# Optimization experiments

Hardware: AMD Instinct MI355X
Metric: run time of the kernel (lower is better)

Reference implementation:

```python
import jax, jax.numpy as jnp
import numpy as np

GRID = 8
SPACING = 2.0
RADIUS = 3.0
B = 64
CODE = 1024
HID = 128
L = 4
EPS = 1e-5


def _layernorm(h, g, b):
    mu = h.mean(-1, keepdims=True)
    var = ((h - mu) ** 2).mean(-1, keepdims=True)
    return (h - mu) * jax.lax.rsqrt(var + EPS) * g + b


def setup_inputs() -> dict:
    key = jax.random.key(0)
    ks = jax.random.split(key, 16)
    n = GRID ** 3
    # grid coords, centered, spacing=anchor_spacing (create_grid_coords)
    idx = np.arange(GRID)
    coords = (np.stack(np.meshgrid(idx, idx, idx, indexing='ij'), -1).reshape(-1, 3)
              - (GRID - 1) / 2.0) * SPACING
    # radius_graph per batch: identical geometry per graph -> offset base edges
    d2 = ((coords[:, None, :] - coords[None, :, :]) ** 2).sum(-1)
    mask = (d2 <= RADIUS ** 2) & (d2 > 0)
    r0, c0 = np.nonzero(mask)
    off = (np.arange(B) * n)[:, None]
    row = (r0[None, :] + off).reshape(-1)
    col = (c0[None, :] + off).reshape(-1)
    edge_index = jnp.asarray(np.stack([row, col]), dtype=jnp.int32)  # [2,E]
    grid_coords = jnp.asarray(np.tile(coords, (B, 1)), dtype=jnp.float32)  # [B*n,3]
    s = 0.02
    inp = {
        'y': jax.random.normal(ks[0], (B, n, CODE), jnp.float32),
        'grid_coords': grid_coords,
        'edge_index': edge_index,
        'W_in': jax.random.normal(ks[1], (HID, CODE), jnp.float32) * s,
        'b_in': jnp.zeros((HID,), jnp.float32),
        'gam': jnp.ones((L, HID), jnp.float32),
        'bet': jnp.zeros((L, HID), jnp.float32),
        'eW1': jax.random.normal(ks[2], (L, HID, 2 * HID + 1), jnp.float32) * s,
        'eb1': jnp.zeros((L, HID), jnp.float32),
        'eW2': jax.random.normal(ks[3], (L, HID, HID), jnp.float32) * s,
        'eb2': jnp.zeros((L, HID), jnp.float32),
        'nW1': jax.random.normal(ks[4], (L, HID, 2 * HID), jnp.float32) * s,
        'nb1': jnp.zeros((L, HID), jnp.float32),
        'nW2': jax.random.normal(ks[5], (L, HID, HID), jnp.float32) * s,
        'nb2': jnp.zeros((L, HID), jnp.float32),
        'W_out': jax.random.normal(ks[6], (CODE, HID), jnp.float32) * s,
        'b_out': jnp.zeros((CODE,), jnp.float32),
    }
    return inp


def reference(y, grid_coords, edge_index, W_in, b_in, gam, bet,
              eW1, eb1, eW2, eb2, nW1, nb1, nW2, nb2, W_out, b_out):
    N = grid_coords.shape[0]  # B*n nodes
    row, col = edge_index[0], edge_index[1]
    rel = grid_coords[col] - grid_coords[row]            # [E,3]
    dist = jnp.linalg.norm(rel, axis=-1, keepdims=True)  # [E,1]
    cnt = jax.ops.segment_sum(jnp.ones((row.shape[0],), y.dtype), col, num_segments=N)
    inv_cnt = jnp.where(cnt > 0, 1.0 / jnp.maximum(cnt, 1.0), 0.0)[:, None]  # [N,1]

    h = jnp.einsum('bnc,hc->bnh', y, W_in) + b_in
    h = h.reshape(N, HID)
    for l in range(L):
        hn = _layernorm(h, gam[l], bet[l])               # [N,H]
        e_in = jnp.concatenate([hn[row], hn[col], dist], axis=-1)  # [E,2H+1]
        m = jax.nn.silu(e_in @ eW1[l].T + eb1[l])
        m = jax.nn.silu(m @ eW2[l].T + eb2[l])           # [E,H]
        m_aggr = jax.ops.segment_sum(m, col, num_segments=N) * inv_cnt  # scatter-mean
        d = jax.nn.silu(jnp.concatenate([hn, m_aggr], axis=-1) @ nW1[l].T + nb1[l])
        d = d @ nW2[l].T + nb2[l]
        h = hn + d                                        # residual on normalized h
    h = h.reshape(B, -1, HID)
    return jnp.einsum('bnh,ch->bnc', h, W_out) + b_out
```

## Files before the change

### kernel.cpp

```cpp
#include <hip/hip_runtime.h>
#include <math.h>


#define HIDDEN 128
#define NLAYERS 4
#define NBASE 512
#define NB 64
#define CODE 1024

typedef __attribute__((ext_vector_type(8))) short s16x8;
typedef __attribute__((ext_vector_type(4))) float f32x4;

__device__ __forceinline__ unsigned int cvt_pk_bf16(float lo, float hi) {
    unsigned int d;
    asm("v_cvt_pk_bf16_f32 %0, %1, %2" : "=v"(d) : "v"(lo), "v"(hi));
    return d;
}
__device__ __forceinline__ unsigned short f2bf(float x) {
    return (unsigned short)cvt_pk_bf16(x, x);
}
__device__ __forceinline__ float silu_f(float x) {
    float e = __expf(-x);
    float r;
    asm("v_rcp_f32 %0, %1" : "=v"(r) : "v"(1.f + e));
    return x * r;
}

__device__ __forceinline__ void conv_body(
    const float* __restrict__ s, unsigned short* __restrict__ d,
    int blk, int tid, int n) {
    int i = (blk * 256 + tid) * 4;
    if (i >= n) return;
    float4 v = *reinterpret_cast<const float4*>(s + i);
    uint2 o = { cvt_pk_bf16(v.x, v.y), cvt_pk_bf16(v.z, v.w) };
    *reinterpret_cast<uint2*>(d + i) = o;
}

__global__ __launch_bounds__(256) void prep_all(
    const float* __restrict__ W_in, const float* __restrict__ W_out,
    const float* __restrict__ nW1, const float* __restrict__ nW2,
    const float* __restrict__ eW2, const float* __restrict__ eW1,
    const float* __restrict__ eb1,
    const int* __restrict__ row, const int* __restrict__ col,
    const float* __restrict__ gc,
    unsigned short* __restrict__ winbf, unsigned short* __restrict__ woutbf,
    unsigned short* __restrict__ wn1bf, unsigned short* __restrict__ wn2bf,
    unsigned short* __restrict__ w2bf, unsigned short* __restrict__ w1ab,
    float* __restrict__ bias256, float* __restrict__ c01,
    int* __restrict__ brp, int* __restrict__ bcol, int baseE) {
    int blk = blockIdx.x, tid = threadIdx.x;
    if (blk < 128)      { conv_body(W_in,  winbf,  blk,       tid, HIDDEN * CODE); return; }
    if (blk < 256)      { conv_body(W_out, woutbf, blk - 128, tid, CODE * HIDDEN); return; }
    if (blk < 384)      { conv_body(nW1,   wn1bf,  blk - 256, tid, NLAYERS * HIDDEN * 256); return; }
    if (blk < 448)      { conv_body(nW2,   wn2bf,  blk - 384, tid, NLAYERS * HIDDEN * HIDDEN); return; }
    if (blk < 512)      { conv_body(eW2,   w2bf,   blk - 448, tid, NLAYERS * HIDDEN * HIDDEN); return; }
    if (blk < 516) {
        int l = blk - 512;
        const float* w = eW1 + (size_t)l * HIDDEN * 257;
        for (int i = tid; i < 256 * 128; i += 256) {
            int n = i >> 7, k = i & 127;
            float v = (n < 128) ? w[(size_t)n * 257 + k]
                                : w[(size_t)(n - 128) * 257 + 128 + k];
            w1ab[(size_t)l * 256 * 128 + i] = f2bf(v);
        }
        if (tid < 256)
            bias256[(size_t)l * 256 + tid] =
                (tid < 128) ? 0.f : eb1[(size_t)l * HIDDEN + tid - 128];
        if (tid < 128) {
            float wd = w[(size_t)tid * 257 + 256];
            c01[(size_t)l * 256 + tid] = 2.f * wd;
            c01[(size_t)l * 256 + 128 + tid] = sqrtf(8.f) * wd;
        }
        return;
    }
    if (blk < 519) {
        int v = (blk - 516) * 256 + tid;
        if (v > NBASE) return;
        int lo = 0, hi = baseE;
        while (lo < hi) {
            int mid = (lo + hi) >> 1;
            if (row[mid] < v) lo = mid + 1; else hi = mid;
        }
        brp[v] = lo;
        return;
    }
    {
        int t = (blk - 519) * 256 + tid;
        if (t >= baseE) return;
        int u = col[t], v = row[t];
        float dx = gc[(size_t)u * 3 + 0] - gc[(size_t)v * 3 + 0];
        float dy = gc[(size_t)u * 3 + 1] - gc[(size_t)v * 3 + 1];
        float dz = gc[(size_t)u * 3 + 2] - gc[(size_t)v * 3 + 2];
        float d2 = dx * dx + dy * dy + dz * dz;
        bcol[t] = u | ((d2 > 6.f ? 1 : 0) << 15);
    }
}

__global__ __launch_bounds__(256) void mgemm64(
    const unsigned short* __restrict__ A, int K,
    const unsigned short* __restrict__ W,
    const float* __restrict__ bias,
    float* __restrict__ Cf, unsigned short* __restrict__ Cb, int ldC, int perm) {
    __shared__ __align__(16) unsigned short As[64 * 128];
    __shared__ __align__(16) unsigned short Ws[128 * 128];
    int tid = threadIdx.x;
    int wid = tid >> 6, l = tid & 63, lr = l & 15, lg = l >> 4;
    int wm = wid >> 1, wn = wid & 1;
    int row0 = blockIdx.x * 64;
    int cb = blockIdx.y * 128;
    f32x4 acc[2][4];
#pragma unroll
    for (int i = 0; i < 2; ++i)
#pragma unroll
        for (int j = 0; j < 4; ++j) {
            f32x4 z = { 0.f, 0.f, 0.f, 0.f };
            acc[i][j] = z;
        }
    for (int kc = 0; kc < K; kc += 128) {
#pragma unroll
        for (int jj = 0; jj < 4; ++jj) {
            int j = tid + jj * 256;
            int r = j >> 4, c = j & 15;
            int srow = row0 + r;
            if (perm == 3) srow = ((srow & 511) << 6) | (srow >> 9);
            s16x8 v = *reinterpret_cast<const s16x8*>(
                A + (size_t)srow * K + kc + c * 8);
            *reinterpret_cast<s16x8*>(&As[r * 128 + ((c ^ (r & 7)) << 3)]) = v;
        }
#pragma unroll
        for (int jj = 0; jj < 8; ++jj) {
            int j = tid + jj * 256;
            int r = j >> 4, c = j & 15;
            s16x8 wv = *reinterpret_cast<const s16x8*>(
                W + (size_t)(cb + r) * K + kc + c * 8);
            *reinterpret_cast<s16x8*>(&Ws[r * 128 + ((c ^ (r & 7)) << 3)]) = wv;
        }
        __syncthreads();
#pragma unroll
        for (int ks = 0; ks < 4; ++ks) {
            int c = ks * 4 + lg;
            s16x8 af[2], bf[4];
#pragma unroll
            for (int mi = 0; mi < 2; ++mi) {
                int r = wm * 32 + mi * 16 + lr;
                af[mi] = *reinterpret_cast<s16x8*>(&As[r * 128 + ((c ^ (r & 7)) << 3)]);
            }
#pragma unroll
            for (int ni = 0; ni < 4; ++ni) {
                int n = wn * 64 + ni * 16 + lr;
                bf[ni] = *reinterpret_cast<s16x8*>(&Ws[n * 128 + ((c ^ (n & 7)) << 3)]);
            }
#pragma unroll
            for (int mi = 0; mi < 2; ++mi)
#pragma unroll
                for (int ni = 0; ni < 4; ++ni)
                    acc[mi][ni] = __builtin_amdgcn_mfma_f32_16x16x32_bf16(
                        af[mi], bf[ni], acc[mi][ni], 0, 0, 0);
        }
        __syncthreads();
    }
#pragma unroll
    for (int mi = 0; mi < 2; ++mi) {
#pragma unroll
        for (int ni = 0; ni < 4; ++ni) {
            int colg = cb + wn * 64 + ni * 16 + lr;
            float bs = bias ? bias[colg] : 0.f;
#pragma unroll
            for (int r4 = 0; r4 < 4; ++r4) {
                int rowg = row0 + wm * 32 + mi * 16 + lg * 4 + r4;
                float v = acc[mi][ni][r4] + bs;
                if (Cf) Cf[(size_t)rowg * ldC + colg] = v;
                if (Cb) Cb[(size_t)rowg * ldC + colg] = f2bf(v);
            }
        }
    }
}

__global__ __launch_bounds__(256) void inproj_ln(
    const float* __restrict__ y,
    const unsigned short* __restrict__ W, const float* __restrict__ bias,
    const float* __restrict__ g, const float* __restrict__ bet,
    float* __restrict__ hn, unsigned short* __restrict__ hnbf) {
    __shared__ __align__(16) unsigned short As[64 * 128];
    __shared__ __align__(16) unsigned short Ws[128 * 128];
    int tid = threadIdx.x;
    int wid = tid >> 6, l = tid & 63, lr = l & 15, lg = l >> 4;
    int row0 = blockIdx.x * 64;
    f32x4 acc[8];
#pragma unroll
    for (int ni = 0; ni < 8; ++ni) {
        f32x4 z = { 0.f, 0.f, 0.f, 0.f };
        acc[ni] = z;
    }
    float4 pa0[4], pa1[4];
    s16x8 pw[8];
    auto loadc = [&](int kc) {
#pragma unroll
        for (int jj = 0; jj < 4; ++jj) {
            int j = tid + jj * 256, r = j >> 4, c = j & 15;
            const float* p = y + (size_t)(row0 + r) * CODE + kc + c * 8;
            pa0[jj] = *reinterpret_cast<const float4*>(p);
            pa1[jj] = *reinterpret_cast<const float4*>(p + 4);
        }
#pragma unroll
        for (int jj = 0; jj < 8; ++jj) {
            int j = tid + jj * 256, r = j >> 4, c = j & 15;
            pw[jj] = *reinterpret_cast<const s16x8*>(W + (size_t)r * CODE + kc + c * 8);
        }
    };
    auto storec = [&]() {
#pragma unroll
        for (int jj = 0; jj < 4; ++jj) {
            int j = tid + jj * 256, r = j >> 4, c = j & 15;
            union { s16x8 s; unsigned int w[4]; } pk;
            pk.w[0] = cvt_pk_bf16(pa0[jj].x, pa0[jj].y);
            pk.w[1] = cvt_pk_bf16(pa0[jj].z, pa0[jj].w);
            pk.w[2] = cvt_pk_bf16(pa1[jj].x, pa1[jj].y);
            pk.w[3] = cvt_pk_bf16(pa1[jj].z, pa1[jj].w);
            *reinterpret_cast<s16x8*>(&As[r * 128 + ((c ^ (r & 7)) << 3)]) = pk.s;
        }
#pragma unroll
        for (int jj = 0; jj < 8; ++jj) {
            int j = tid + jj * 256, r = j >> 4, c = j & 15;
            *reinterpret_cast<s16x8*>(&Ws[r * 128 + ((c ^ (r & 7)) << 3)]) = pw[jj];
        }
    };
    loadc(0);
    for (int kc8 = 0; kc8 < 8; ++kc8) {
        storec();
        __syncthreads();
        if (kc8 < 7) loadc((kc8 + 1) * 128);
#pragma unroll
        for (int ks = 0; ks < 4; ++ks) {
            int c = ks * 4 + lg;
            int r = wid * 16 + lr;
            s16x8 af = *reinterpret_cast<s16x8*>(&As[r * 128 + ((c ^ (r & 7)) << 3)]);
#pragma unroll
            for (int ni = 0; ni < 8; ++ni) {
                int n = ni * 16 + lr;
                s16x8 bf = *reinterpret_cast<s16x8*>(&Ws[n * 128 + ((c ^ (n & 7)) << 3)]);
                acc[ni] = __builtin_amdgcn_mfma_f32_16x16x32_bf16(af, bf, acc[ni], 0, 0, 0);
            }
        }
        __syncthreads();
    }
#pragma unroll
    for (int ni = 0; ni < 8; ++ni) {
        float bs = bias[ni * 16 + lr];
#pragma unroll
        for (int r4 = 0; r4 < 4; ++r4) acc[ni][r4] += bs;
    }
    float s[4], q[4];
#pragma unroll
    for (int r4 = 0; r4 < 4; ++r4) {
        float ss = 0.f, qq = 0.f;
#pragma unroll
        for (int ni = 0; ni < 8; ++ni) {
            float v = acc[ni][r4];
            ss += v; qq += v * v;
        }
#pragma unroll
        for (int o = 1; o < 16; o <<= 1) {
            ss += __shfl_xor(ss, o, 64);
            qq += __shfl_xor(qq, o, 64);
        }
        float mu = ss * (1.f / 128.f);
        float var = qq * (1.f / 128.f) - mu * mu;
        s[r4] = mu;
        q[r4] = rsqrtf(var + 1e-5f);
    }
#pragma unroll
    for (int ni = 0; ni < 8; ++ni) {
        int col = ni * 16 + lr;
        float gg = g[col], bb = bet[col];
#pragma unroll
        for (int r4 = 0; r4 < 4; ++r4) {
            int rowg = row0 + wid * 16 + lg * 4 + r4;
            int orow = (rowg & 511) * 64 + (rowg >> 9);
            float o = (acc[ni][r4] - s[r4]) * q[r4] * gg + bb;
            hn[(size_t)orow * HIDDEN + col] = o;
            hnbf[(size_t)orow * HIDDEN + col] = f2bf(o);
        }
    }
}

__global__ __launch_bounds__(256) void nmlp_ln(
    const unsigned short* __restrict__ hnbf,
    const unsigned short* __restrict__ magbf,
    const unsigned short* __restrict__ w1, const float* __restrict__ b1,
    const unsigned short* __restrict__ w2, const float* __restrict__ b2,
    const float* __restrict__ resid,
    const float* __restrict__ g, const float* __restrict__ bet,
    float* __restrict__ hn_out, unsigned short* __restrict__ hnbf_out,
    unsigned short* __restrict__ hbf_out,
    const unsigned short* __restrict__ w1ab_next,
    const float* __restrict__ eb1_next,
    unsigned short* __restrict__ ab_out) {
    __shared__ __align__(16) unsigned short As[64 * 128];
    __shared__ __align__(16) unsigned short Ws[128 * 128];
    int tid = threadIdx.x;
    int wid = tid >> 6, l = tid & 63, lr = l & 15, lg = l >> 4;
    int row0 = blockIdx.x * 64;
    f32x4 acc[8];
#pragma unroll
    for (int ni = 0; ni < 8; ++ni) {
        f32x4 z = { 0.f, 0.f, 0.f, 0.f };
        acc[ni] = z;
    }
    for (int kc = 0; kc < 2; ++kc) {
        const unsigned short* Xsrc = kc ? magbf : hnbf;
#pragma unroll
        for (int jj = 0; jj < 4; ++jj) {
            int j = tid + jj * 256;
            int r = j >> 4, c = j & 15;
            s16x8 v = *reinterpret_cast<const s16x8*>(
                Xsrc + (size_t)(row0 + r) * 128 + c * 8);
            *reinterpret_cast<s16x8*>(&As[r * 128 + ((c ^ (r & 7)) << 3)]) = v;
        }
#pragma unroll
        for (int jj = 0; jj < 8; ++jj) {
            int j = tid + jj * 256;
            int r = j >> 4, c = j & 15;
            s16x8 wv = *reinterpret_cast<const s16x8*>(
                w1 + (size_t)r * 256 + kc * 128 + c * 8);
            *reinterpret_cast<s16x8*>(&Ws[r * 128 + ((c ^ (r & 7)) << 3)]) = wv;
        }
        __syncthreads();
#pragma unroll
        for (int ks = 0; ks < 4; ++ks) {
            int c = ks * 4 + lg;
            int r = wid * 16 + lr;
            s16x8 af = *reinterpret_cast<s16x8*>(&As[r * 128 + ((c ^ (r & 7)) << 3)]);
#pragma unroll
            for (int ni = 0; ni < 8; ++ni) {
                int n = ni * 16 + lr;
                s16x8 bf = *reinterpret_cast<s16x8*>(&Ws[n * 128 + ((c ^ (n & 7)) << 3)]);
                acc[ni] = __builtin_amdgcn_mfma_f32_16x16x32_bf16(af, bf, acc[ni], 0, 0, 0);
            }
        }
        __syncthreads();
    }
#pragma unroll
    for (int ni = 0; ni < 8; ++ni) {
        int col = ni * 16 + lr;
        float bs = b1[col];
        int cc = col >> 3, cin = col & 7;
#pragma unroll
        for (int r4 = 0; r4 < 4; ++r4) {
            int rl = wid * 16 + lg * 4 + r4;
            As[rl * 128 + ((cc ^ (rl & 7)) << 3) + cin] =
                f2bf(silu_f(acc[ni][r4] + bs));
            acc[ni][r4] = 0.f;
        }
    }
#pragma unroll
    for (int jj = 0; jj < 8; ++jj) {
        int j = tid + jj * 256;
        int r = j >> 4, c = j & 15;
        s16x8 wv = *reinterpret_cast<const s16x8*>(w2 + (size_t)r * 128 + c * 8);
        *reinterpret_cast<s16x8*>(&Ws[r * 128 + ((c ^ (r & 7)) << 3)]) = wv;
    }
    __syncthreads();
#pragma unroll
    for (int ks = 0; ks < 4; ++ks) {
        int c = ks * 4 + lg;
        int r = wid * 16 + lr;
        s16x8 af = *reinterpret_cast<s16x8*>(&As[r * 128 + ((c ^ (r & 7)) << 3)]);
#pragma unroll
        for (int ni = 0; ni < 8; ++ni) {
            int n = ni * 16 + lr;
            s16x8 bf = *reinterpret_cast<s16x8*>(&Ws[n * 128 + ((c ^ (n & 7)) << 3)]);
            acc[ni] = __builtin_amdgcn_mfma_f32_16x16x32_bf16(af, bf, acc[ni], 0, 0, 0);
        }
    }
#pragma unroll
    for (int ni = 0; ni < 8; ++ni) {
        int col = ni * 16 + lr;
        float bs = b2[col];
#pragma unroll
        for (int r4 = 0; r4 < 4; ++r4) {
            int rowg = row0 + wid * 16 + lg * 4 + r4;
            acc[ni][r4] += bs + resid[(size_t)rowg * HIDDEN + col];
        }
    }
    if (!g) {
#pragma unroll
        for (int ni = 0; ni < 8; ++ni) {
            int col = ni * 16 + lr;
#pragma unroll
            for (int r4 = 0; r4 < 4; ++r4) {
                int rowg = row0 + wid * 16 + lg * 4 + r4;
                hbf_out[(size_t)rowg * HIDDEN + col] = f2bf(acc[ni][r4]);
            }
        }
        return;
    }
    float s[4], q[4];
#pragma unroll
    for (int r4 = 0; r4 < 4; ++r4) {
        float ss = 0.f, qq = 0.f;
#pragma unroll
        for (int ni = 0; ni < 8; ++ni) {
            float v = acc[ni][r4];
            ss += v; qq += v * v;
        }
#pragma unroll
        for (int o = 1; o < 16; o <<= 1) {
            ss += __shfl_xor(ss, o, 64);
            qq += __shfl_xor(qq, o, 64);
        }
        float mu = ss * (1.f / 128.f);
        float var = qq * (1.f / 128.f) - mu * mu;
        s[r4] = mu;
        q[r4] = rsqrtf(var + 1e-5f);
    }
#pragma unroll
    for (int ni = 0; ni < 8; ++ni) {
        int col = ni * 16 + lr;
        float gg = g[col], bb = bet[col];
#pragma unroll
        for (int r4 = 0; r4 < 4; ++r4) {
            int rowg = row0 + wid * 16 + lg * 4 + r4;
            float o = (acc[ni][r4] - s[r4]) * q[r4] * gg + bb;
            hn_out[(size_t)rowg * HIDDEN + col] = o;
            hnbf_out[(size_t)rowg * HIDDEN + col] = f2bf(o);
            acc[ni][r4] = o;
        }
    }
#pragma unroll
    for (int ni = 0; ni < 8; ++ni) {
        int col = ni * 16 + lr;
        int cc = col >> 3, cin = col & 7;
#pragma unroll
        for (int r4 = 0; r4 < 4; ++r4) {
            int rl = wid * 16 + lg * 4 + r4;
            As[rl * 128 + ((cc ^ (rl & 7)) << 3) + cin] = f2bf(acc[ni][r4]);
        }
    }
    __syncthreads();
#pragma unroll
    for (int half = 0; half < 2; ++half) {
#pragma unroll
        for (int jj = 0; jj < 8; ++jj) {
            int j = tid + jj * 256;
            int r = j >> 4, c = j & 15;
            s16x8 wv = *reinterpret_cast<const s16x8*>(
                w1ab_next + (size_t)(half * 128 + r) * 128 + c * 8);
            *reinterpret_cast<s16x8*>(&Ws[r * 128 + ((c ^ (r & 7)) << 3)]) = wv;
        }
        __syncthreads();
#pragma unroll
        for (int ni = 0; ni < 8; ++ni) {
            f32x4 z = { 0.f, 0.f, 0.f, 0.f };
            acc[ni] = z;
        }
#pragma unroll
        for (int ks = 0; ks < 4; ++ks) {
            int c = ks * 4 + lg;
            int r = wid * 16 + lr;
            s16x8 af = *reinterpret_cast<s16x8*>(&As[r * 128 + ((c ^ (r & 7)) << 3)]);
#pragma unroll
            for (int ni = 0; ni < 8; ++ni) {
                int n = ni * 16 + lr;
                s16x8 bf = *reinterpret_cast<s16x8*>(&Ws[n * 128 + ((c ^ (n & 7)) << 3)]);
                acc[ni] = __builtin_amdgcn_mfma_f32_16x16x32_bf16(af, bf, acc[ni], 0, 0, 0);
            }
        }
#pragma unroll
        for (int ni = 0; ni < 8; ++ni) {
            int col = ni * 16 + lr;
            float bs = half ? eb1_next[col] : 0.f;
#pragma unroll
            for (int r4 = 0; r4 < 4; ++r4) {
                int rowg = row0 + wid * 16 + lg * 4 + r4;
                ab_out[(size_t)rowg * 256 + half * 128 + col] =
                    f2bf(acc[ni][r4] + bs);
            }
        }
        if (half == 0) __syncthreads();
    }
}

__global__ __launch_bounds__(256, 4) void edge_mfma7(
    const unsigned short* __restrict__ ABbf,
    const int* __restrict__ bcol,
    const int* __restrict__ brp,
    const unsigned short* __restrict__ w2bf,
    const float* __restrict__ c01,
    const float* __restrict__ eb2l,
    unsigned short* __restrict__ magbf) {
    __shared__ __align__(16) unsigned short m1[2][16 * 128];
    int tid = threadIdx.x;
    int blk = blockIdx.x;
    int i = blk >> 2, qtr = blk & 3;
    int wid = tid >> 6, l = tid & 63, lr = l & 15, lg = l >> 4;
    int rowb = qtr * 16;
    int col0 = wid * 32;

    s16x8 wfr[4][2];
#pragma unroll
    for (int ks = 0; ks < 4; ++ks)
#pragma unroll
        for (int ni = 0; ni < 2; ++ni) {
            int n = col0 + ni * 16 + lr;
            wfr[ks][ni] = *reinterpret_cast<const s16x8*>(
                w2bf + (size_t)n * 128 + (ks * 4 + lg) * 8);
        }

    int s = brp[i], e = brp[i + 1];

    int br = tid >> 4, bc = tid & 15;
    s16x8 Bp[2];
    {
        union { s16x8 s; unsigned int w[4]; } bv;
        bv.s = *reinterpret_cast<const s16x8*>(
            ABbf + ((size_t)i * NB + rowb + br) * 256 + 128 + bc * 8);
#pragma unroll
        for (int cls = 0; cls < 2; ++cls) {
            const float* cp = c01 + cls * 128 + bc * 8;
            float4 ca = *reinterpret_cast<const float4*>(cp);
            float4 cb = *reinterpret_cast<const float4*>(cp + 4);
            union { s16x8 s; unsigned int w[4]; } pk;
            pk.w[0] = cvt_pk_bf16(__uint_as_float(bv.w[0] << 16) + ca.x,
                                  __uint_as_float(bv.w[0] & 0xffff0000u) + ca.y);
            pk.w[1] = cvt_pk_bf16(__uint_as_float(bv.w[1] << 16) + ca.z,
                                  __uint_as_float(bv.w[1] & 0xffff0000u) + ca.w);
            pk.w[2] = cvt_pk_bf16(__uint_as_float(bv.w[2] << 16) + cb.x,
                                  __uint_as_float(bv.w[2] & 0xffff0000u) + cb.y);
            pk.w[3] = cvt_pk_bf16(__uint_as_float(bv.w[3] << 16) + cb.z,
                                  __uint_as_float(bv.w[3] & 0xffff0000u) + cb.w);
            Bp[cls] = pk.s;
        }
    }
    float e2[2], se[2];
#pragma unroll
    for (int ni = 0; ni < 2; ++ni) {
        e2[ni] = eb2l[col0 + ni * 16 + lr];
        se[ni] = silu_f(e2[ni]);
    }
    f32x4 agg[2];
#pragma unroll
    for (int ni = 0; ni < 2; ++ni) {
        f32x4 z = { 0.f, 0.f, 0.f, 0.f };
        agg[ni] = z;
    }

    int pk0 = __builtin_amdgcn_readfirstlane(bcol[s]);
    s16x8 Areg = *reinterpret_cast<const s16x8*>(
        ABbf + ((size_t)(pk0 & 0x7fff) * NB + rowb + br) * 256 + bc * 8);

    for (int t = s; t < e; ++t) {
        int cls = (pk0 >> 15) & 1;
        int pkn = pk0;
        s16x8 An = Areg;
        if (t + 1 < e) {
            pkn = __builtin_amdgcn_readfirstlane(bcol[t + 1]);
            An = *reinterpret_cast<const s16x8*>(
                ABbf + ((size_t)(pkn & 0x7fff) * NB + rowb + br) * 256 + bc * 8);
        }
        {
            union { s16x8 s; unsigned int w[4]; } av, bv2, pkv;
            av.s = Areg;
            bv2.s = cls ? Bp[1] : Bp[0];
#pragma unroll
            for (int q = 0; q < 4; ++q) {
                float a0 = __uint_as_float(av.w[q] << 16);
                float a1 = __uint_as_float(av.w[q] & 0xffff0000u);
                float b0 = __uint_as_float(bv2.w[q] << 16);
                float b1 = __uint_as_float(bv2.w[q] & 0xffff0000u);
                pkv.w[q] = cvt_pk_bf16(silu_f(a0 + b0), silu_f(a1 + b1));
            }
            *reinterpret_cast<s16x8*>(
                &m1[t & 1][br * 128 + ((bc ^ (br & 7)) << 3)]) = pkv.s;
        }
        __syncthreads();
        f32x4 acc[2];
#pragma unroll
        for (int ni = 0; ni < 2; ++ni) {
            f32x4 iv = { e2[ni], e2[ni], e2[ni], e2[ni] };
            acc[ni] = iv;
        }
#pragma unroll
        for (int ks = 0; ks < 4; ++ks) {
            int cc = ks * 4 + lg;
            s16x8 af = *reinterpret_cast<s16x8*>(
                &m1[t & 1][lr * 128 + ((cc ^ (lr & 7)) << 3)]);
            acc[0] = __builtin_amdgcn_mfma_f32_16x16x32_bf16(af, wfr[ks][0], acc[0], 0, 0, 0);
            acc[1] = __builtin_amdgcn_mfma_f32_16x16x32_bf16(af, wfr[ks][1], acc[1], 0, 0, 0);
        }
#pragma unroll
        for (int ni = 0; ni < 2; ++ni)
#pragma unroll
            for (int r4 = 0; r4 < 4; ++r4)
                agg[ni][r4] += silu_f(acc[ni][r4]) - se[ni];
        pk0 = pkn;
        Areg = An;
    }

    float inv = (e > s) ? 1.f / (float)(e - s) : 0.f;
#pragma unroll
    for (int ni = 0; ni < 2; ++ni) {
#pragma unroll
        for (int r4 = 0; r4 < 4; ++r4) {
            size_t rowg = (size_t)i * NB + rowb + lg * 4 + r4;
            magbf[rowg * 128 + col0 + ni * 16 + lr] =
                f2bf(agg[ni][r4] * inv + se[ni]);
        }
    }
}

extern "C" void kernel_launch(void* const* d_in, const int* in_sizes, int n_in,
                              void* d_out, int out_size, void* d_ws, size_t ws_size,
                              hipStream_t stream) {
    const float* y     = (const float*)d_in[0];
    const float* gc    = (const float*)d_in[1];
    const int*   eidx  = (const int*)d_in[2];
    const float* W_in  = (const float*)d_in[3];
    const float* b_in  = (const float*)d_in[4];
    const float* gam   = (const float*)d_in[5];
    const float* bet   = (const float*)d_in[6];
    const float* eW1   = (const float*)d_in[7];
    const float* eb1   = (const float*)d_in[8];
    const float* eW2   = (const float*)d_in[9];
    const float* eb2   = (const float*)d_in[10];
    const float* nW1   = (const float*)d_in[11];
    const float* nb1   = (const float*)d_in[12];
    const float* nW2   = (const float*)d_in[13];
    const float* nb2   = (const float*)d_in[14];
    const float* W_out = (const float*)d_in[15];
    const float* b_out = (const float*)d_in[16];

    const int M = in_sizes[0] / CODE;
    const int E = in_sizes[2] / 2;
    const int baseE = E / NB;

    float* out = (float*)d_out;

    char* ws = (char*)d_ws;
    size_t off = 0;
    auto carve = [&](size_t bytes) {
        char* p = ws + off;
        off += (bytes + 255) & ~(size_t)255;
        return p;
    };
    float*          buf_hn  = (float*)carve((size_t)M * HIDDEN * 4);
    unsigned short* hnbf    = (unsigned short*)carve((size_t)M * HIDDEN * 2);
    unsigned short* ABbf    = (unsigned short*)carve((size_t)M * 256 * 2);
    unsigned short* magbf   = (unsigned short*)carve((size_t)M * HIDDEN * 2);
    unsigned short* hbf     = (unsigned short*)carve((size_t)M * HIDDEN * 2);
    int*            brp     = (int*)carve((size_t)(NBASE + 1) * 4);
    int*            bcol    = (int*)carve((size_t)baseE * 4);
    unsigned short* winbf   = (unsigned short*)carve((size_t)HIDDEN * CODE * 2);
    unsigned short* woutbf  = (unsigned short*)carve((size_t)CODE * HIDDEN * 2);
    unsigned short* wn1bf   = (unsigned short*)carve((size_t)NLAYERS * HIDDEN * 256 * 2);
    unsigned short* wn2bf   = (unsigned short*)carve((size_t)NLAYERS * HIDDEN * HIDDEN * 2);
    unsigned short* w2bf    = (unsigned short*)carve((size_t)NLAYERS * HIDDEN * HIDDEN * 2);
    unsigned short* w1ab    = (unsigned short*)carve((size_t)NLAYERS * 256 * HIDDEN * 2);
    float*          bias256 = (float*)carve((size_t)NLAYERS * 256 * 4);
    float*          c01     = (float*)carve((size_t)NLAYERS * 256 * 4);

    const int* row  = eidx;
    const int* colA = eidx + E;

    int prep_blocks = 519 + (baseE + 255) / 256;
    prep_all<<<dim3(prep_blocks), 256, 0, stream>>>(
        W_in, W_out, nW1, nW2, eW2, eW1, eb1, row, colA, gc,
        winbf, woutbf, wn1bf, wn2bf, w2bf, w1ab, bias256, c01,
        brp, bcol, baseE);

    inproj_ln<<<dim3(M / 64), 256, 0, stream>>>(
        y, winbf, b_in, gam, bet, buf_hn, hnbf);

    mgemm64<<<dim3(M / 64, 2), 256, 0, stream>>>(
        hnbf, HIDDEN, w1ab, bias256, nullptr, ABbf, 256, 0);

    for (int l = 0; l < NLAYERS; ++l) {
        edge_mfma7<<<dim3(NBASE * 4), 256, 0, stream>>>(
            ABbf, bcol, brp,
            w2bf + (size_t)l * HIDDEN * HIDDEN, c01 + (size_t)l * 256,
            eb2 + (size_t)l * HIDDEN, magbf);

        bool last = (l == NLAYERS - 1);
        nmlp_ln<<<dim3(M / 64), 256, 0, stream>>>(
            hnbf, magbf,
            wn1bf + (size_t)l * HIDDEN * 256, nb1 + (size_t)l * HIDDEN,
            wn2bf + (size_t)l * HIDDEN * HIDDEN, nb2 + (size_t)l * HIDDEN,
            buf_hn,
            last ? nullptr : gam + (size_t)(l + 1) * HIDDEN,
            last ? nullptr : bet + (size_t)(l + 1) * HIDDEN,
            buf_hn, hnbf, hbf,
            last ? nullptr : w1ab + (size_t)(l + 1) * 256 * HIDDEN,
            last ? nullptr : eb1 + (size_t)(l + 1) * HIDDEN,
            last ? nullptr : ABbf);
    }

    mgemm64<<<dim3(M / 64, CODE / 128), 256, 0, stream>>>(
        hbf, HIDDEN, woutbf, b_out, out, nullptr, CODE, 3);
}
```

Before: 455.3 us.

## Fuse layer-0 edge projection into inproj, pair edges in edge kernel

The first-layer AB projection GEMM (hn times w1ab plus eb1 bias) moves into the epilogue of the input-projection/LayerNorm kernel, which removes one launch and one round trip of hn through memory. The bias256 buffer goes away because the bias is applied inline. The edge kernel now handles two edges per barrier using four shared buffers and prefetches two edges ahead, which halves the number of __syncthreads. The node MLP reads its A fragments straight from global memory instead of staging them in LDS. These changes add register and LDS pressure, and the direct global A loads may be uncoalesced.

```diff
diff --git a/kernel.cpp b/kernel.cpp
--- a/kernel.cpp
+++ b/kernel.cpp
@@ -46,7 +46,7 @@
     unsigned short* __restrict__ winbf, unsigned short* __restrict__ woutbf,
     unsigned short* __restrict__ wn1bf, unsigned short* __restrict__ wn2bf,
     unsigned short* __restrict__ w2bf, unsigned short* __restrict__ w1ab,
-    float* __restrict__ bias256, float* __restrict__ c01,
+    float* __restrict__ c01,
     int* __restrict__ brp, int* __restrict__ bcol, int baseE) {
     int blk = blockIdx.x, tid = threadIdx.x;
     if (blk < 128)      { conv_body(W_in,  winbf,  blk,       tid, HIDDEN * CODE); return; }
@@ -63,9 +63,6 @@
                                 : w[(size_t)(n - 128) * 257 + 128 + k];
             w1ab[(size_t)l * 256 * 128 + i] = f2bf(v);
         }
-        if (tid < 256)
-            bias256[(size_t)l * 256 + tid] =
-                (tid < 128) ? 0.f : eb1[(size_t)l * HIDDEN + tid - 128];
         if (tid < 128) {
             float wd = w[(size_t)tid * 257 + 256];
             c01[(size_t)l * 256 + tid] = 2.f * wd;
@@ -180,7 +177,10 @@
     const float* __restrict__ y,
     const unsigned short* __restrict__ W, const float* __restrict__ bias,
     const float* __restrict__ g, const float* __restrict__ bet,
-    float* __restrict__ hn, unsigned short* __restrict__ hnbf) {
+    float* __restrict__ hn, unsigned short* __restrict__ hnbf,
+    const unsigned short* __restrict__ w1ab0,
+    const float* __restrict__ eb1_0,
+    unsigned short* __restrict__ ab_out) {
     __shared__ __align__(16) unsigned short As[64 * 128];
     __shared__ __align__(16) unsigned short Ws[128 * 128];
     int tid = threadIdx.x;
@@ -269,18 +269,65 @@
         s[r4] = mu;
         q[r4] = rsqrtf(var + 1e-5f);
     }
+    int orow_[4];
 #pragma unroll
     for (int ni = 0; ni < 8; ++ni) {
         int col = ni * 16 + lr;
         float gg = g[col], bb = bet[col];
+        int cc = col >> 3, cin = col & 7;
 #pragma unroll
         for (int r4 = 0; r4 < 4; ++r4) {
             int rowg = row0 + wid * 16 + lg * 4 + r4;
             int orow = (rowg & 511) * 64 + (rowg >> 9);
+            orow_[r4] = orow;
             float o = (acc[ni][r4] - s[r4]) * q[r4] * gg + bb;
             hn[(size_t)orow * HIDDEN + col] = o;
             hnbf[(size_t)orow * HIDDEN + col] = f2bf(o);
-        }
+            int rl = wid * 16 + lg * 4 + r4;
+            As[rl * 128 + ((cc ^ (rl & 7)) << 3) + cin] = f2bf(o);
+        }
+    }
+#pragma unroll
+    for (int half = 0; half < 2; ++half) {
+#pragma unroll
+        for (int jj = 0; jj < 8; ++jj) {
+            int j = tid + jj * 256;
+            int r = j >> 4, c = j & 15;
+            s16x8 wv = *reinterpret_cast<const s16x8*>(
+                w1ab0 + (size_t)(half * 128 + r) * 128 + c * 8);
+            *reinterpret_cast<s16x8*>(&Ws[r * 128 + ((c ^ (r & 7)) << 3)]) = wv;
+        }
+        __syncthreads();
+#pragma unroll
+        for (int ni = 0; ni < 8; ++ni) {
+            f32x4 z = { 0.f, 0.f, 0.f, 0.f };
+            acc[ni] = z;
+        }
+#pragma unroll
+        for (int ks = 0; ks < 4; ++ks) {
+            int c = ks * 4 + lg;
+            int r = wid * 16 + lr;
+            s16x8 af = *reinterpret_cast<s16x8*>(&As[r * 128 + ((c ^ (r & 7)) << 3)]);
+#pragma unroll
+            for (int ni = 0; ni < 8; ++ni) {
+                int n = ni * 16 + lr;
+                s16x8 bf = *reinterpret_cast<s16x8*>(&Ws[n * 128 + ((c ^ (n & 7)) << 3)]);
+                acc[ni] = __builtin_amdgcn_mfma_f32_16x16x32_bf16(af, bf, acc[ni], 0, 0, 0);
+            }
+        }
+#pragma unroll
+        for (int ni = 0; ni < 8; ++ni) {
+            int col = ni * 16 + lr;
+            float bs = half ? eb1_0[col] : 0.f;
+#pragma unroll
+            for (int r4 = 0; r4 < 4; ++r4) {
+                int rowg = row0 + wid * 16 + lg * 4 + r4;
+                int orow = (rowg & 511) * 64 + (rowg >> 9);
+                ab_out[(size_t)orow * 256 + half * 128 + col] =
+                    f2bf(acc[ni][r4] + bs);
+            }
+        }
+        if (half == 0) __syncthreads();
     }
 }
 
@@ -301,6 +348,7 @@
     int tid = threadIdx.x;
     int wid = tid >> 6, l = tid & 63, lr = l & 15, lg = l >> 4;
     int row0 = blockIdx.x * 64;
+    int myrow = row0 + wid * 16 + lr;
     f32x4 acc[8];
 #pragma unroll
     for (int ni = 0; ni < 8; ++ni) {
@@ -309,14 +357,6 @@
     }
     for (int kc = 0; kc < 2; ++kc) {
         const unsigned short* Xsrc = kc ? magbf : hnbf;
-#pragma unroll
-        for (int jj = 0; jj < 4; ++jj) {
-            int j = tid + jj * 256;
-            int r = j >> 4, c = j & 15;
-            s16x8 v = *reinterpret_cast<const s16x8*>(
-                Xsrc + (size_t)(row0 + r) * 128 + c * 8);
-            *reinterpret_cast<s16x8*>(&As[r * 128 + ((c ^ (r & 7)) << 3)]) = v;
-        }
 #pragma unroll
         for (int jj = 0; jj < 8; ++jj) {
             int j = tid + jj * 256;
@@ -328,12 +368,12 @@
         __syncthreads();
 #pragma unroll
         for (int ks = 0; ks < 4; ++ks) {
-            int c = ks * 4 + lg;
-            int r = wid * 16 + lr;
-            s16x8 af = *reinterpret_cast<s16x8*>(&As[r * 128 + ((c ^ (r & 7)) << 3)]);
+            s16x8 af = *reinterpret_cast<const s16x8*>(
+                Xsrc + (size_t)myrow * 128 + ks * 32 + lg * 8);
 #pragma unroll
             for (int ni = 0; ni < 8; ++ni) {
                 int n = ni * 16 + lr;
+                int c = ks * 4 + lg;
                 s16x8 bf = *reinterpret_cast<s16x8*>(&Ws[n * 128 + ((c ^ (n & 7)) << 3)]);
                 acc[ni] = __builtin_amdgcn_mfma_f32_16x16x32_bf16(af, bf, acc[ni], 0, 0, 0);
             }
@@ -418,23 +458,15 @@
     for (int ni = 0; ni < 8; ++ni) {
         int col = ni * 16 + lr;
         float gg = g[col], bb = bet[col];
+        int cc = col >> 3, cin = col & 7;
 #pragma unroll
         for (int r4 = 0; r4 < 4; ++r4) {
             int rowg = row0 + wid * 16 + lg * 4 + r4;
             float o = (acc[ni][r4] - s[r4]) * q[r4] * gg + bb;
             hn_out[(size_t)rowg * HIDDEN + col] = o;
             hnbf_out[(size_t)rowg * HIDDEN + col] = f2bf(o);
-            acc[ni][r4] = o;
-        }
-    }
-#pragma unroll
-    for (int ni = 0; ni < 8; ++ni) {
-        int col = ni * 16 + lr;
-        int cc = col >> 3, cin = col & 7;
-#pragma unroll
-        for (int r4 = 0; r4 < 4; ++r4) {
             int rl = wid * 16 + lg * 4 + r4;
-            As[rl * 128 + ((cc ^ (rl & 7)) << 3) + cin] = f2bf(acc[ni][r4]);
+            As[rl * 128 + ((cc ^ (rl & 7)) << 3) + cin] = f2bf(o);
         }
     }
     __syncthreads();
@@ -481,7 +513,7 @@
     }
 }
 
-__global__ __launch_bounds__(256, 4) void edge_mfma7(
+__global__ __launch_bounds__(256, 4) void edge_mfma8(
     const unsigned short* __restrict__ ABbf,
     const int* __restrict__ bcol,
     const int* __restrict__ brp,
@@ -489,7 +521,7 @@
     const float* __restrict__ c01,
     const float* __restrict__ eb2l,
     unsigned short* __restrict__ magbf) {
-    __shared__ __align__(16) unsigned short m1[2][16 * 128];
+    __shared__ __align__(16) unsigned short m1[4][16 * 128];
     int tid = threadIdx.x;
     int blk = blockIdx.x;
     int i = blk >> 2, qtr = blk & 3;
@@ -508,7 +540,6 @@
         }
 
     int s = brp[i], e = brp[i + 1];
-
     int br = tid >> 4, bc = tid & 15;
     s16x8 Bp[2];
     {
@@ -545,35 +576,27 @@
         agg[ni] = z;
     }
 
-    int pk0 = __builtin_amdgcn_readfirstlane(bcol[s]);
-    s16x8 Areg = *reinterpret_cast<const s16x8*>(
-        ABbf + ((size_t)(pk0 & 0x7fff) * NB + rowb + br) * 256 + bc * 8);
-
-    for (int t = s; t < e; ++t) {
-        int cls = (pk0 >> 15) & 1;
-        int pkn = pk0;
-        s16x8 An = Areg;
-        if (t + 1 < e) {
-            pkn = __builtin_amdgcn_readfirstlane(bcol[t + 1]);
-            An = *reinterpret_cast<const s16x8*>(
-                ABbf + ((size_t)(pkn & 0x7fff) * NB + rowb + br) * 256 + bc * 8);
-        }
-        {
-            union { s16x8 s; unsigned int w[4]; } av, bv2, pkv;
-            av.s = Areg;
-            bv2.s = cls ? Bp[1] : Bp[0];
-#pragma unroll
-            for (int q = 0; q < 4; ++q) {
-                float a0 = __uint_as_float(av.w[q] << 16);
-                float a1 = __uint_as_float(av.w[q] & 0xffff0000u);
-                float b0 = __uint_as_float(bv2.w[q] << 16);
-                float b1 = __uint_as_float(bv2.w[q] & 0xffff0000u);
-                pkv.w[q] = cvt_pk_bf16(silu_f(a0 + b0), silu_f(a1 + b1));
-            }
-            *reinterpret_cast<s16x8*>(
-                &m1[t & 1][br * 128 + ((bc ^ (br & 7)) << 3)]) = pkv.s;
-        }
-        __syncthreads();
+    auto loadA = [&](int t, int& pk) -> s16x8 {
+        pk = __builtin_amdgcn_readfirstlane(bcol[t]);
+        return *reinterpret_cast<const s16x8*>(
+            ABbf + ((size_t)(pk & 0x7fff) * NB + rowb + br) * 256 + bc * 8);
+    };
+    auto build = [&](s16x8 A, int cls, int buf) {
+        union { s16x8 s; unsigned int w[4]; } av, bv2, pkv;
+        av.s = A;
+        bv2.s = cls ? Bp[1] : Bp[0];
+#pragma unroll
+        for (int q = 0; q < 4; ++q) {
+            float a0 = __uint_as_float(av.w[q] << 16);
+            float a1 = __uint_as_float(av.w[q] & 0xffff0000u);
+            float b0 = __uint_as_float(bv2.w[q] << 16);
+            float b1 = __uint_as_float(bv2.w[q] & 0xffff0000u);
+            pkv.w[q] = cvt_pk_bf16(silu_f(a0 + b0), silu_f(a1 + b1));
+        }
+        *reinterpret_cast<s16x8*>(
+            &m1[buf][br * 128 + ((bc ^ (br & 7)) << 3)]) = pkv.s;
+    };
+    auto mfma_epi = [&](int buf) {
         f32x4 acc[2];
 #pragma unroll
         for (int ni = 0; ni < 2; ++ni) {
@@ -584,7 +607,7 @@
         for (int ks = 0; ks < 4; ++ks) {
             int cc = ks * 4 + lg;
             s16x8 af = *reinterpret_cast<s16x8*>(
-                &m1[t & 1][lr * 128 + ((cc ^ (lr & 7)) << 3)]);
+                &m1[buf][lr * 128 + ((cc ^ (lr & 7)) << 3)]);
             acc[0] = __builtin_amdgcn_mfma_f32_16x16x32_bf16(af, wfr[ks][0], acc[0], 0, 0, 0);
             acc[1] = __builtin_amdgcn_mfma_f32_16x16x32_bf16(af, wfr[ks][1], acc[1], 0, 0, 0);
         }
@@ -593,8 +616,27 @@
 #pragma unroll
             for (int r4 = 0; r4 < 4; ++r4)
                 agg[ni][r4] += silu_f(acc[ni][r4]) - se[ni];
-        pk0 = pkn;
-        Areg = An;
+    };
+
+    int pk0, pk1;
+    s16x8 A0 = loadA(s, pk0);
+    s16x8 A1 = A0;
+    pk1 = pk0;
+    if (s + 1 < e) A1 = loadA(s + 1, pk1);
+
+    for (int t = s; t < e; t += 2) {
+        int pb = (((t - s) >> 1) & 1) << 1;
+        bool has2 = (t + 1) < e;
+        int pk2 = pk0, pk3 = pk1;
+        s16x8 A2 = A0, A3 = A1;
+        if (t + 2 < e) A2 = loadA(t + 2, pk2);
+        if (t + 3 < e) A3 = loadA(t + 3, pk3);
+        build(A0, (pk0 >> 15) & 1, pb);
+        if (has2) build(A1, (pk1 >> 15) & 1, pb + 1);
+        __syncthreads();
+        mfma_epi(pb);
+        if (has2) mfma_epi(pb + 1);
+        pk0 = pk2; A0 = A2; pk1 = pk3; A1 = A3;
     }
 
     float inv = (e > s) ? 1.f / (float)(e - s) : 0.f;
@@ -656,7 +698,6 @@
     unsigned short* wn2bf   = (unsigned short*)carve((size_t)NLAYERS * HIDDEN * HIDDEN * 2);
     unsigned short* w2bf    = (unsigned short*)carve((size_t)NLAYERS * HIDDEN * HIDDEN * 2);
     unsigned short* w1ab    = (unsigned short*)carve((size_t)NLAYERS * 256 * HIDDEN * 2);
-    float*          bias256 = (float*)carve((size_t)NLAYERS * 256 * 4);
     float*          c01     = (float*)carve((size_t)NLAYERS * 256 * 4);
 
     const int* row  = eidx;
@@ -665,17 +706,14 @@
     int prep_blocks = 519 + (baseE + 255) / 256;
     prep_all<<<dim3(prep_blocks), 256, 0, stream>>>(
         W_in, W_out, nW1, nW2, eW2, eW1, eb1, row, colA, gc,
-        winbf, woutbf, wn1bf, wn2bf, w2bf, w1ab, bias256, c01,
+        winbf, woutbf, wn1bf, wn2bf, w2bf, w1ab, c01,
         brp, bcol, baseE);
 
     inproj_ln<<<dim3(M / 64), 256, 0, stream>>>(
-        y, winbf, b_in, gam, bet, buf_hn, hnbf);
-
-    mgemm64<<<dim3(M / 64, 2), 256, 0, stream>>>(
-        hnbf, HIDDEN, w1ab, bias256, nullptr, ABbf, 256, 0);
+        y, winbf, b_in, gam, bet, buf_hn, hnbf, w1ab, eb1, ABbf);
 
     for (int l = 0; l < NLAYERS; ++l) {
-        edge_mfma7<<<dim3(NBASE * 4), 256, 0, stream>>>(
+        edge_mfma8<<<dim3(NBASE * 4), 256, 0, stream>>>(
             ABbf, bcol, brp,
             w2bf + (size_t)l * HIDDEN * HIDDEN, c01 + (size_t)l * 256,
             eb2 + (size_t)l * HIDDEN, magbf);
```

Result: faster. 437.9 us (-3.8%).
